# Performance work log

Hardware: AMD Instinct MI355X
Metric: run time of the kernel (lower is better)

Reference implementation:

```python
import jax, jax.numpy as jnp
import numpy as np

Na, Np, F, C, H, L, OUT = 50000, 100000, 128, 128, 8, 2, 64
D = C // H  # head dim = 16
E = 150000


def setup_inputs() -> dict:
    key = jax.random.key(0)
    ks = jax.random.split(key, 16)
    p = lambda k, shape: jax.random.normal(k, shape, jnp.float32) * 0.05
    return {
        "x_author": jax.random.normal(ks[0], (Na, F), jnp.float32),
        "x_paper": jax.random.normal(ks[1], (Np, F), jnp.float32),
        # per-node-type input projections (HGT.lin_dict)
        "win_w": p(ks[2], (2, F, C)), "win_b": p(ks[3], (2, C)),
        # per-layer, per-node-type K/Q/V linears of HGTConv
        "kqv_w": p(ks[4], (L, 2, 3, C, C)), "kqv_b": p(ks[5], (L, 2, 3, C)),
        # per-layer, per-node-type output linear a_lin
        "a_w": p(ks[6], (L, 2, C, C)), "a_b": p(ks[7], (L, 2, C)),
        # per-layer, per-node-type skip gate (init 1 like PyG)
        "skip": jnp.ones((L, 2), jnp.float32),
        # per-layer, per-edge-type relation matrices a_rel/m_rel and prior p_rel
        "rel_a": p(ks[8], (L, 2, H, D, D)), "rel_m": p(ks[9], (L, 2, H, D, D)),
        "rel_p": jnp.ones((L, 2, H), jnp.float32),
        # final classifier on author nodes
        "out_w": p(ks[10], (C, OUT)), "out_b": p(ks[11], (OUT,)),
        # edge type 0: author -> paper ('writes'); edge type 1: paper -> author (reverse)
        "ei_writes_src": jax.random.randint(ks[12], (E,), 0, Na, jnp.int32),
        "ei_writes_dst": jax.random.randint(ks[13], (E,), 0, Np, jnp.int32),
        "ei_rev_src": jax.random.randint(ks[14], (E,), 0, Np, jnp.int32),
        "ei_rev_dst": jax.random.randint(ks[15], (E,), 0, Na, jnp.int32),
    }


def _segment_softmax(alpha, dst, n):
    # softmax of alpha [E, H] over edges grouped by destination node (PyG softmax)
    m = jnp.full((n, alpha.shape[1]), -jnp.inf, alpha.dtype).at[dst].max(alpha)
    ex = jnp.exp(alpha - m[dst])
    s = jnp.zeros((n, alpha.shape[1]), alpha.dtype).at[dst].add(ex)
    return ex / (s[dst] + 1e-16)


def _hgt_forward(x_author, x_paper, win_w, win_b, kqv_w, kqv_b, a_w, a_b,
                 skip, rel_a, rel_m, rel_p, out_w, out_b, ei):
    # per-node-type input linear + relu
    xs = [jax.nn.relu(x_author @ win_w[0] + win_b[0]),
          jax.nn.relu(x_paper @ win_w[1] + win_b[1])]
    edge_types = [(0, 1, ei[0], ei[1]),  # author -> paper
                  (1, 0, ei[2], ei[3])]  # paper -> author
    nl = kqv_w.shape[0]
    inv_sqrt_d = np.float32(1.0 / np.sqrt(D))
    for l in range(nl):
        # K/Q/V per node type, shape [N_t, H, D]
        kqv = [[(xs[t] @ kqv_w[l, t, i] + kqv_b[l, t, i]).reshape(-1, H, D)
                for i in range(3)] for t in range(2)]
        agg = [jnp.zeros((xs[t].shape[0], H, D), xs[t].dtype) for t in range(2)]
        for e, (st, dt, src, dst) in enumerate(edge_types):
            # relation-specific transforms at node level, then gather at edges
            kn = jnp.einsum('nhd,hde->nhe', kqv[st][0], rel_a[l, e])
            vn = jnp.einsum('nhd,hde->nhe', kqv[st][2], rel_m[l, e])
            alpha = jnp.einsum('ehd,ehd->eh', kqv[dt][1][dst], kn[src])
            alpha = alpha * rel_p[l, e] * inv_sqrt_d
            alpha = _segment_softmax(alpha, dst, xs[dt].shape[0])
            agg[dt] = agg[dt].at[dst].add(alpha[:, :, None] * vn[src])
        new_xs = []
        for t in range(2):
            o = jax.nn.gelu(agg[t].reshape(-1, C), approximate=False)
            o = o @ a_w[l, t] + a_b[l, t]
            g = jax.nn.sigmoid(skip[l, t])
            new_xs.append(g * o + (1.0 - g) * xs[t])  # skip connection (dims match)
        xs = new_xs
    return xs[0] @ out_w + out_b  # author output


def reference(x_author, x_paper, win_w, win_b, kqv_w, kqv_b, a_w, a_b, skip,
              rel_a, rel_m, rel_p, out_w, out_b,
              ei_writes_src, ei_writes_dst, ei_rev_src, ei_rev_dst):
    ei = (ei_writes_src, ei_writes_dst, ei_rev_src, ei_rev_dst)
    return _hgt_forward(x_author, x_paper, win_w, win_b, kqv_w, kqv_b,
                        a_w, a_b, skip, rel_a, rel_m, rel_p, out_w, out_b, ei)
```

## Files before the change

### kernel.cpp

```cpp
#include <hip/hip_runtime.h>
#include <math.h>

namespace {

constexpr int Na = 50000, Np = 100000, L = 2, E = 150000;
constexpr int SCAN_TILE = 2048;

typedef __attribute__((ext_vector_type(8))) short short8v;
typedef __attribute__((ext_vector_type(4))) float f32x4;

__device__ inline float geluf(float x){ return 0.5f*x*(1.0f + erff(x*0.7071067811865476f)); }

__device__ inline float bf2f(unsigned short u){ return __uint_as_float(((unsigned)u) << 16); }
__device__ inline unsigned short f2bf(float f){
  unsigned u = __float_as_uint(f);
  u += 0x7FFFu + ((u >> 16) & 1u);
  return (unsigned short)(u >> 16);
}
__device__ inline unsigned pk2(float a, float b){
  return (unsigned)f2bf(a) | ((unsigned)f2bf(b) << 16);
}

struct StF32 {
  using T = float;
  static __device__ float ld(const T* p){ return *p; }
  static __device__ short8v ld8(const T* __restrict__ p){
    float4 lo = *reinterpret_cast<const float4*>(p);
    float4 hi = *reinterpret_cast<const float4*>(p+4);
    short8v v;
    v[0]=(short)f2bf(lo.x); v[1]=(short)f2bf(lo.y); v[2]=(short)f2bf(lo.z); v[3]=(short)f2bf(lo.w);
    v[4]=(short)f2bf(hi.x); v[5]=(short)f2bf(hi.y); v[6]=(short)f2bf(hi.z); v[7]=(short)f2bf(hi.w);
    return v;
  }
};
struct StBF16 {
  using T = unsigned short;
  static __device__ float ld(const T* p){ return bf2f(*p); }
  static __device__ short8v ld8(const T* __restrict__ p){
    return *reinterpret_cast<const short8v*>(p);
  }
  static __device__ void ld16(const T* __restrict__ p, float* o){
    const uint4* q = reinterpret_cast<const uint4*>(p);
    #pragma unroll
    for (int half = 0; half < 2; ++half){
      uint4 u = q[half];
      o[half*8+0] = bf2f((unsigned short)(u.x & 0xffff));
      o[half*8+1] = bf2f((unsigned short)(u.x >> 16));
      o[half*8+2] = bf2f((unsigned short)(u.y & 0xffff));
      o[half*8+3] = bf2f((unsigned short)(u.y >> 16));
      o[half*8+4] = bf2f((unsigned short)(u.z & 0xffff));
      o[half*8+5] = bf2f((unsigned short)(u.z >> 16));
      o[half*8+6] = bf2f((unsigned short)(u.w & 0xffff));
      o[half*8+7] = bf2f((unsigned short)(u.w >> 16));
    }
  }
};

__global__ void zero_int_kernel(int* __restrict__ p, int n){
  int i = blockIdx.x*256 + threadIdx.x;
  int stride = gridDim.x*256;
  for (; i < n; i += stride) p[i] = 0;
}

__global__ void diag_kernel(float* o, float v){
  if (threadIdx.x == 0 && blockIdx.x == 0) o[0] = v;
}

__global__ void hist_kernel(const int* __restrict__ dst, int* __restrict__ counts, int nE){
  int e = blockIdx.x*256 + threadIdx.x;
  if (e >= nE) return;
  atomicAdd(&counts[dst[e]], 1);
}

__global__ void scan_a(const int* __restrict__ counts, int* __restrict__ bsum, int n){
  int base = blockIdx.x*SCAN_TILE;
  int s = 0;
  for (int i = threadIdx.x; i < SCAN_TILE; i += 256){
    int g = base + i;
    s += (g < n) ? counts[g] : 0;
  }
  __shared__ int red[256];
  red[threadIdx.x] = s;
  __syncthreads();
  for (int off = 128; off > 0; off >>= 1){
    if (threadIdx.x < off) red[threadIdx.x] += red[threadIdx.x + off];
    __syncthreads();
  }
  if (threadIdx.x == 0) bsum[blockIdx.x] = red[0];
}

__global__ void scan_b(int* __restrict__ bsum, int nb){
  __shared__ int sh[1024];
  int t = threadIdx.x;
  int v = (t < nb) ? bsum[t] : 0;
  sh[t] = v;
  __syncthreads();
  for (int off = 1; off < 1024; off <<= 1){
    int add = (t >= off) ? sh[t-off] : 0;
    __syncthreads();
    sh[t] += add;
    __syncthreads();
  }
  if (t < nb) bsum[t] = sh[t] - v;
}

__global__ void scan_c(int* __restrict__ counts, const int* __restrict__ bsum,
                       int* __restrict__ rp, int n){
  int base = blockIdx.x*SCAN_TILE;
  __shared__ int sh[SCAN_TILE];
  for (int i = threadIdx.x; i < SCAN_TILE; i += 256){
    int g = base + i;
    sh[i] = (g < n) ? counts[g] : 0;
  }
  __syncthreads();
  int t = threadIdx.x;
  int loc[8], s = 0;
  #pragma unroll
  for (int i = 0; i < 8; ++i){ loc[i] = s; s += sh[t*8 + i]; }
  __shared__ int red[256];
  red[t] = s;
  __syncthreads();
  for (int off = 1; off < 256; off <<= 1){
    int add = (t >= off) ? red[t-off] : 0;
    __syncthreads();
    red[t] += add;
    __syncthreads();
  }
  int texcl = red[t] - s + bsum[blockIdx.x];
  #pragma unroll
  for (int i = 0; i < 8; ++i){
    int g = base + t*8 + i;
    if (g < n){
      int v = texcl + loc[i];
      rp[g] = v;
      counts[g] = v;
      if (g == n-1) rp[n] = v + sh[t*8 + i];
    }
  }
}

__global__ void fill_slots_kernel(const int* __restrict__ src, const int* __restrict__ dst,
                                  int* __restrict__ cursor, int* __restrict__ slots, int nE){
  int e = blockIdx.x*256 + threadIdx.x;
  if (e >= nE) return;
  int slot = atomicAdd(&cursor[dst[e]], 1);
  slots[slot] = src[e];
}

__global__ void eff_w_kernel(const float* __restrict__ kqv_w, const float* __restrict__ kqv_b,
                             const float* __restrict__ rel_a, const float* __restrict__ rel_m,
                             float* __restrict__ effw, float* __restrict__ effb){
  int idx = blockIdx.x*256 + threadIdx.x;
  if (idx >= 2*2*2*128*128) return;
  int j = idx & 127; int f = (idx >> 7) & 127; int c = idx >> 14;
  int kv = c & 1, t = (c >> 1) & 1, l = c >> 2;
  int h = j >> 4, e2 = j & 15;
  int i = (kv == 0) ? 0 : 2;
  const float* W = kqv_w + ((size_t)(((l*2 + t)*3 + i)*128) + f)*128 + h*16;
  const float* A = ((kv == 0) ? rel_a : rel_m) + ((size_t)(l*2 + t)*8 + h)*256;
  float acc = 0.f;
  #pragma unroll
  for (int d = 0; d < 16; ++d) acc += W[d]*A[d*16 + e2];
  effw[(size_t)c*16384 + f*128 + j] = acc;
  if (f == 0){
    const float* B = kqv_b + (size_t)((l*2 + t)*3 + i)*128 + h*16;
    float ab = 0.f;
    #pragma unroll
    for (int d = 0; d < 16; ++d) ab += B[d]*A[d*16 + e2];
    effb[c*128 + j] = ab;
  }
}

struct PrepSrc { const float* s[19]; };
__global__ void prep_w_kernel(PrepSrc P, unsigned short* __restrict__ wbf){
  int idx = blockIdx.x*256 + threadIdx.x;
  if (idx >= 19*16384) return;
  int s = idx >> 14, j = idx & 16383;
  int n = j >> 7, k = j & 127;
  int nc = (s == 18) ? 64 : 128;
  if (n >= nc) return;
  wbf[(size_t)s*16384 + n*128 + k] = f2bf(P.s[s][(size_t)k*nc + n]);
}

__device__ inline void stage_w(short* Bs, const unsigned short* __restrict__ WT, int t, int rows){
  for (int c = t; c < rows*16; c += 256){
    int r = c >> 4, c16 = c & 15;
    short8v v = *reinterpret_cast<const short8v*>(&WT[r*128 + c16*8]);
    *reinterpret_cast<short8v*>(&Bs[r*128 + ((c16 ^ (r&7))<<3)]) = v;
  }
}

template<int BN, int GELU_IN, int RELU_OUT, int SKIP, typename SIn>
__global__ __launch_bounds__(256) void gemm_kernel(
    const typename SIn::T* __restrict__ X,
    const unsigned short* __restrict__ WT,
    const float* __restrict__ bias,
    void* __restrict__ Y, int N,
    const unsigned short* __restrict__ skip_x,
    const float* __restrict__ skip_s)
{
  __shared__ __align__(16) short As[128*128];
  __shared__ __align__(16) char Braw[32768];
  short* Bs = (short*)Braw;
  const int t = threadIdx.x;
  const int row0 = blockIdx.x*128;
  for (int c = t; c < 128*16; c += 256){
    int r = c >> 4, c16 = c & 15;
    int gr = row0 + r;
    short8v v;
    if (gr < N){
      v = SIn::ld8(&X[(size_t)gr*128 + c16*8]);
      if (GELU_IN){
        #pragma unroll
        for (int i = 0; i < 8; ++i){
          float f = geluf(bf2f((unsigned short)v[i]));
          v[i] = (short)f2bf(f);
        }
      }
    } else {
      v = (short8v)0;
    }
    *reinterpret_cast<short8v*>(&As[r*128 + ((c16 ^ (r&7))<<3)]) = v;
  }
  stage_w(Bs, WT, t, BN);
  __syncthreads();
  const int lane = t & 63, wid = t >> 6;
  const int wm = wid >> 1, wn = wid & 1;
  constexpr int NR = BN/32;
  const int lr = lane & 15, lk = lane >> 4;
  f32x4 acc[4][NR] = {};
  #pragma unroll
  for (int kk = 0; kk < 4; ++kk){
    int kc = kk*4 + lk;
    short8v a[4], b[NR];
    #pragma unroll
    for (int m = 0; m < 4; ++m){
      int r = wm*64 + m*16 + lr;
      a[m] = *reinterpret_cast<const short8v*>(&As[r*128 + ((kc ^ (r&7))<<3)]);
    }
    #pragma unroll
    for (int n = 0; n < NR; ++n){
      int col = wn*(BN/2) + n*16 + lr;
      b[n] = *reinterpret_cast<const short8v*>(&Bs[col*128 + ((kc ^ (col&7))<<3)]);
    }
    #pragma unroll
    for (int m = 0; m < 4; ++m)
      #pragma unroll
      for (int n = 0; n < NR; ++n)
        acc[m][n] = __builtin_amdgcn_mfma_f32_16x16x32_bf16(b[n], a[m], acc[m][n], 0, 0, 0);
  }
  __syncthreads();

  if constexpr (BN == 128){
    #pragma unroll
    for (int m = 0; m < 4; ++m){
      int row = wm*64 + m*16 + lr;
      #pragma unroll
      for (int n = 0; n < NR; ++n){
        int col0 = wn*64 + n*16 + lk*4;
        float4 b4 = *reinterpret_cast<const float4*>(&bias[col0]);
        float y0 = acc[m][n][0] + b4.x, y1 = acc[m][n][1] + b4.y;
        float y2 = acc[m][n][2] + b4.z, y3 = acc[m][n][3] + b4.w;
        if (RELU_OUT){
          y0 = fmaxf(y0,0.f); y1 = fmaxf(y1,0.f); y2 = fmaxf(y2,0.f); y3 = fmaxf(y3,0.f);
        }
        uint2 pk; pk.x = pk2(y0,y1); pk.y = pk2(y2,y3);
        int c16 = col0 >> 3;
        *reinterpret_cast<uint2*>(&Bs[row*128 + ((c16 ^ (row&7))<<3) + (col0&7)]) = pk;
      }
    }
    __syncthreads();
    float g = 1.f, og = 0.f;
    if (SKIP){ float sv = *skip_s; g = 1.f/(1.f + expf(-sv)); og = 1.f - g; }
    unsigned short* out = (unsigned short*)Y;
    for (int c = t; c < 128*16; c += 256){
      int r = c >> 4, c16 = c & 15;
      int gr = row0 + r;
      if (gr >= N) continue;
      short8v v = *reinterpret_cast<const short8v*>(&Bs[r*128 + ((c16 ^ (r&7))<<3)]);
      if (SKIP){
        short8v s8 = *reinterpret_cast<const short8v*>(&skip_x[(size_t)gr*128 + c16*8]);
        short8v o8;
        #pragma unroll
        for (int i = 0; i < 8; ++i)
          o8[i] = (short)f2bf(g*bf2f((unsigned short)v[i]) + og*bf2f((unsigned short)s8[i]));
        *reinterpret_cast<short8v*>(&out[(size_t)gr*128 + c16*8]) = o8;
      } else {
        *reinterpret_cast<short8v*>(&out[(size_t)gr*128 + c16*8]) = v;
      }
    }
  } else {
    float* Bf = (float*)Braw;
    #pragma unroll
    for (int m = 0; m < 4; ++m){
      int row = wm*64 + m*16 + lr;
      #pragma unroll
      for (int n = 0; n < NR; ++n){
        int col0 = wn*32 + n*16 + lk*4;
        float4 b4 = *reinterpret_cast<const float4*>(&bias[col0]);
        float4 y;
        y.x = acc[m][n][0] + b4.x; y.y = acc[m][n][1] + b4.y;
        y.z = acc[m][n][2] + b4.z; y.w = acc[m][n][3] + b4.w;
        int cf = col0 >> 2;
        *reinterpret_cast<float4*>(&Bf[row*64 + ((cf ^ (row&7))<<2)]) = y;
      }
    }
    __syncthreads();
    float* out = (float*)Y;
    for (int c = t; c < 128*16; c += 256){
      int r = c >> 4, cf = c & 15;
      int gr = row0 + r;
      if (gr >= N) continue;
      float4 v = *reinterpret_cast<const float4*>(&Bf[r*64 + ((cf ^ (r&7))<<2)]);
      *reinterpret_cast<float4*>(&out[(size_t)gr*64 + cf*4]) = v;
    }
  }
}

__global__ __launch_bounds__(256) void qkv_kernel(
    const unsigned short* __restrict__ X,
    const unsigned short* __restrict__ WTq,
    const unsigned short* __restrict__ WTk,
    const unsigned short* __restrict__ WTv,
    const float* __restrict__ bq, const float* __restrict__ bk, const float* __restrict__ bv,
    unsigned short* __restrict__ Q, unsigned short* __restrict__ K, unsigned short* __restrict__ V,
    int N)
{
  __shared__ __align__(16) short As[128*128];
  __shared__ __align__(16) short Bs[128*128];
  const int t = threadIdx.x;
  const int row0 = blockIdx.x*128;
  for (int c = t; c < 128*16; c += 256){
    int r = c >> 4, c16 = c & 15;
    int gr = row0 + r;
    short8v v = (gr < N) ? *reinterpret_cast<const short8v*>(&X[(size_t)gr*128 + c16*8])
                         : (short8v)0;
    *reinterpret_cast<short8v*>(&As[r*128 + ((c16 ^ (r&7))<<3)]) = v;
  }
  const int lane = t & 63, wid = t >> 6;
  const int wm = wid >> 1, wn = wid & 1;
  const int lr = lane & 15, lk = lane >> 4;
  const unsigned short* wts[3] = {WTq, WTk, WTv};
  const float* bias[3] = {bq, bk, bv};
  unsigned short* outs[3] = {Q, K, V};
  #pragma unroll
  for (int s = 0; s < 3; ++s){
    __syncthreads();
    stage_w(Bs, wts[s], t, 128);
    __syncthreads();
    f32x4 acc[4][4] = {};
    #pragma unroll
    for (int kk = 0; kk < 4; ++kk){
      int kc = kk*4 + lk;
      short8v a[4], b[4];
      #pragma unroll
      for (int m = 0; m < 4; ++m){
        int r = wm*64 + m*16 + lr;
        a[m] = *reinterpret_cast<const short8v*>(&As[r*128 + ((kc ^ (r&7))<<3)]);
      }
      #pragma unroll
      for (int n = 0; n < 4; ++n){
        int col = wn*64 + n*16 + lr;
        b[n] = *reinterpret_cast<const short8v*>(&Bs[col*128 + ((kc ^ (col&7))<<3)]);
      }
      #pragma unroll
      for (int m = 0; m < 4; ++m)
        #pragma unroll
        for (int n = 0; n < 4; ++n)
          acc[m][n] = __builtin_amdgcn_mfma_f32_16x16x32_bf16(b[n], a[m], acc[m][n], 0, 0, 0);
    }
    __syncthreads();
    const float* bi = bias[s];
    #pragma unroll
    for (int m = 0; m < 4; ++m){
      int row = wm*64 + m*16 + lr;
      #pragma unroll
      for (int n = 0; n < 4; ++n){
        int col0 = wn*64 + n*16 + lk*4;
        float4 b4 = *reinterpret_cast<const float4*>(&bi[col0]);
        uint2 pk;
        pk.x = pk2(acc[m][n][0] + b4.x, acc[m][n][1] + b4.y);
        pk.y = pk2(acc[m][n][2] + b4.z, acc[m][n][3] + b4.w);
        int c16 = col0 >> 3;
        *reinterpret_cast<uint2*>(&Bs[row*128 + ((c16 ^ (row&7))<<3) + (col0&7)]) = pk;
      }
    }
    __syncthreads();
    unsigned short* out = outs[s];
    for (int c = t; c < 128*16; c += 256){
      int r = c >> 4, c16 = c & 15;
      int gr = row0 + r;
      if (gr >= N) continue;
      short8v v = *reinterpret_cast<const short8v*>(&Bs[r*128 + ((c16 ^ (r&7))<<3)]);
      *reinterpret_cast<short8v*>(&out[(size_t)gr*128 + c16*8]) = v;
    }
  }
}

__global__ void attn_gather_kernel(unsigned short* __restrict__ QA,
                                   const unsigned short* __restrict__ K,
                                   const unsigned short* __restrict__ V,
                                   const int* __restrict__ rp, const int* __restrict__ slots,
                                   const float* __restrict__ relp, int N){
  int idx = blockIdx.x*256 + threadIdx.x;
  if (idx >= N*8) return;
  int h = idx & 7, n = idx >> 3;
  float q[16];
  StBF16::ld16(&QA[(size_t)n*128 + h*16], q);
  float scale_h = relp[h]*0.25f;
  float m = -INFINITY, s = 0.f, acc[16];
  #pragma unroll
  for (int i = 0; i < 16; ++i) acc[i] = 0.f;
  int b = rp[n], e = rp[n+1];
  for (int j = b; j < e; ++j){
    int sv = slots[j];
    float kf[16], vf[16];
    StBF16::ld16(&K[(size_t)sv*128 + h*16], kf);
    float a = 0.f;
    #pragma unroll
    for (int i = 0; i < 16; ++i) a += q[i]*kf[i];
    a *= scale_h;
    float mn = fmaxf(m, a);
    float c = expf(m - mn);
    float p = expf(a - mn);
    StBF16::ld16(&V[(size_t)sv*128 + h*16], vf);
    s = s*c + p;
    #pragma unroll
    for (int i = 0; i < 16; ++i) acc[i] = acc[i]*c + p*vf[i];
    m = mn;
  }
  float inv = 1.f/(s + 1e-16f);
  #pragma unroll
  for (int i = 0; i < 16; ++i) QA[(size_t)n*128 + h*16 + i] = f2bf(acc[i]*inv);
}

struct Ptrs {
  const float *x_author, *x_paper, *win_w, *win_b, *kqv_w, *kqv_b, *a_w, *a_b;
  const float *skip, *rel_a, *rel_m, *rel_p, *out_w, *out_b;
  const int *src0, *dst0, *src1, *dst1;
};

static void run_pipeline(const Ptrs& P, float* d_out, char* ws, hipStream_t stream){
  using BF = unsigned short;
  size_t off = 0;
  auto alloc = [&](size_t bytes) -> void* {
    void* p = ws + off;
    off += (bytes + 255) & ~(size_t)255;
    return p;
  };
  BF* X0 = (BF*)alloc((size_t)Na*128*2);
  BF* X1 = (BF*)alloc((size_t)Np*128*2);
  BF* Q0 = (BF*)alloc((size_t)Na*128*2);
  BF* Q1 = (BF*)alloc((size_t)Np*128*2);
  BF* K0 = (BF*)alloc((size_t)Na*128*2);
  BF* K1 = (BF*)alloc((size_t)Np*128*2);
  BF* V0 = (BF*)alloc((size_t)Na*128*2);
  BF* V1 = (BF*)alloc((size_t)Np*128*2);
  float* effw = (float*)alloc((size_t)8*16384*4);
  float* effb = (float*)alloc((size_t)8*128*4);
  BF* wbf = (BF*)alloc((size_t)19*16384*2);
  int* rp0   = (int*)alloc((size_t)(Np+1)*4);
  int* cur0  = (int*)alloc((size_t)Np*4);
  int* slot0 = (int*)alloc((size_t)E*4);
  int* rp1   = (int*)alloc((size_t)(Na+1)*4);
  int* cur1  = (int*)alloc((size_t)Na*4);
  int* slot1 = (int*)alloc((size_t)E*4);
  int* bsum  = (int*)alloc((size_t)1024*4);

  auto cdiv = [](int a, int b){ return (a+b-1)/b; };
  const int geE = cdiv(E, 256);
  const int ga = cdiv(Na, 128), gp = cdiv(Np, 128);
  const int sb0 = cdiv(Np, SCAN_TILE), sb1 = cdiv(Na, SCAN_TILE);

  eff_w_kernel<<<512, 256, 0, stream>>>(P.kqv_w, P.kqv_b, P.rel_a, P.rel_m, effw, effb);

  PrepSrc ps;
  ps.s[0] = P.win_w; ps.s[1] = P.win_w + 16384;
  for (int l = 0; l < 2; ++l)
    for (int t = 0; t < 2; ++t){
      ps.s[2 + l*2 + t]  = P.kqv_w + (size_t)((l*2+t)*3+1)*16384;
      ps.s[6 + l*2 + t]  = effw + (size_t)(l*4+t*2+0)*16384;
      ps.s[10 + l*2 + t] = effw + (size_t)(l*4+t*2+1)*16384;
      ps.s[14 + l*2 + t] = P.a_w + (size_t)(l*2+t)*16384;
    }
  ps.s[18] = P.out_w;
  prep_w_kernel<<<cdiv(19*16384,256),256,0,stream>>>(ps, wbf);

  zero_int_kernel<<<512,256,0,stream>>>(cur0, Np);
  zero_int_kernel<<<512,256,0,stream>>>(cur1, Na);
  hist_kernel<<<geE,256,0,stream>>>(P.dst0, cur0, E);
  hist_kernel<<<geE,256,0,stream>>>(P.dst1, cur1, E);
  scan_a<<<sb0,256,0,stream>>>(cur0, bsum, Np);
  scan_b<<<1,1024,0,stream>>>(bsum, sb0);
  scan_c<<<sb0,256,0,stream>>>(cur0, bsum, rp0, Np);
  scan_a<<<sb1,256,0,stream>>>(cur1, bsum, Na);
  scan_b<<<1,1024,0,stream>>>(bsum, sb1);
  scan_c<<<sb1,256,0,stream>>>(cur1, bsum, rp1, Na);
  fill_slots_kernel<<<geE,256,0,stream>>>(P.src0, P.dst0, cur0, slot0, E);
  fill_slots_kernel<<<geE,256,0,stream>>>(P.src1, P.dst1, cur1, slot1, E);

  auto W = [&](int s){ return wbf + (size_t)s*16384; };

  gemm_kernel<128,0,1,0,StF32><<<ga,256,0,stream>>>(P.x_author, W(0), P.win_b,     X0, Na, nullptr, nullptr);
  gemm_kernel<128,0,1,0,StF32><<<gp,256,0,stream>>>(P.x_paper,  W(1), P.win_b+128, X1, Np, nullptr, nullptr);

  for (int l = 0; l < L; ++l){
    qkv_kernel<<<ga,256,0,stream>>>(X0, W(2+l*2+0), W(6+l*2+0), W(10+l*2+0),
                                    P.kqv_b + ((l*2+0)*3+1)*128, effb + (l*4+0)*128, effb + (l*4+1)*128,
                                    Q0, K0, V0, Na);
    qkv_kernel<<<gp,256,0,stream>>>(X1, W(2+l*2+1), W(6+l*2+1), W(10+l*2+1),
                                    P.kqv_b + ((l*2+1)*3+1)*128, effb + (l*4+2)*128, effb + (l*4+3)*128,
                                    Q1, K1, V1, Np);
    attn_gather_kernel<<<cdiv(Np*8,256),256,0,stream>>>(Q1, K0, V0, rp0, slot0, P.rel_p + (l*2+0)*8, Np);
    attn_gather_kernel<<<cdiv(Na*8,256),256,0,stream>>>(Q0, K1, V1, rp1, slot1, P.rel_p + (l*2+1)*8, Na);
    gemm_kernel<128,1,0,1,StBF16><<<ga,256,0,stream>>>(Q0, W(14+l*2+0), P.a_b + (l*2+0)*128, X0, Na, X0, P.skip + (l*2+0));
    gemm_kernel<128,1,0,1,StBF16><<<gp,256,0,stream>>>(Q1, W(14+l*2+1), P.a_b + (l*2+1)*128, X1, Np, X1, P.skip + (l*2+1));
  }

  gemm_kernel<64,0,0,0,StBF16><<<ga,256,0,stream>>>(X0, W(18), P.out_b, d_out, Na, nullptr, nullptr);
}

static size_t plan_bytes(){
  auto al = [](size_t x){ return (x + 255) & ~(size_t)255; };
  size_t t = 0;
  t += 4*(al((size_t)Na*128*2) + al((size_t)Np*128*2));
  t += al((size_t)8*16384*4) + al((size_t)8*128*4) + al((size_t)19*16384*2);
  t += al((size_t)(Np+1)*4) + al((size_t)Np*4) + al((size_t)E*4);
  t += al((size_t)(Na+1)*4) + al((size_t)Na*4) + al((size_t)E*4);
  t += al((size_t)1024*4);
  return t;
}

}

extern "C" void kernel_launch(void* const* d_in, const int* in_sizes, int n_in,
                              void* d_out, int out_size, void* d_ws, size_t ws_size,
                              hipStream_t stream){
  Ptrs P;
  P.x_author = (const float*)d_in[0];
  P.x_paper  = (const float*)d_in[1];
  P.win_w = (const float*)d_in[2];
  P.win_b = (const float*)d_in[3];
  P.kqv_w = (const float*)d_in[4];
  P.kqv_b = (const float*)d_in[5];
  P.a_w   = (const float*)d_in[6];
  P.a_b   = (const float*)d_in[7];
  P.skip  = (const float*)d_in[8];
  P.rel_a = (const float*)d_in[9];
  P.rel_m = (const float*)d_in[10];
  P.rel_p = (const float*)d_in[11];
  P.out_w = (const float*)d_in[12];
  P.out_b = (const float*)d_in[13];
  P.src0 = (const int*)d_in[14];
  P.dst0 = (const int*)d_in[15];
  P.src1 = (const int*)d_in[16];
  P.dst1 = (const int*)d_in[17];

  if (ws_size >= plan_bytes()){
    run_pipeline(P, (float*)d_out, (char*)d_ws, stream);
  } else {
    diag_kernel<<<1,1,0,stream>>>((float*)d_out, (float)((double)ws_size/1.0e6));
  }
}
```

Measured before the change: 394.7 us.

## Merge per-node-type launches into grouped kernels and use 512-thread GEMM blocks

Each pair of per-node-type launches (input GEMM, QKV, attention gather, output GEMM) becomes one grouped launch that picks its part from the block index through argument structs. This cuts the launch count and lets the small author-type work fill the device alongside the paper-type work. The GEMM and QKV kernels also move from 4 to 8 waves per 128-row tile, each wave holding half the accumulators. That raises occupancy per block but leaves less MFMA work per wave, and the large LDS tile per block still limits how many blocks fit on a CU.

```diff
diff --git a/kernel.cpp b/kernel.cpp
--- a/kernel.cpp
+++ b/kernel.cpp
@@ -23,7 +23,6 @@
 
 struct StF32 {
   using T = float;
-  static __device__ float ld(const T* p){ return *p; }
   static __device__ short8v ld8(const T* __restrict__ p){
     float4 lo = *reinterpret_cast<const float4*>(p);
     float4 hi = *reinterpret_cast<const float4*>(p+4);
@@ -35,7 +34,6 @@
 };
 struct StBF16 {
   using T = unsigned short;
-  static __device__ float ld(const T* p){ return bf2f(*p); }
   static __device__ short8v ld8(const T* __restrict__ p){
     return *reinterpret_cast<const short8v*>(p);
   }
@@ -183,28 +181,39 @@
 }
 
 __device__ inline void stage_w(short* Bs, const unsigned short* __restrict__ WT, int t, int rows){
-  for (int c = t; c < rows*16; c += 256){
+  for (int c = t; c < rows*16; c += 512){
     int r = c >> 4, c16 = c & 15;
     short8v v = *reinterpret_cast<const short8v*>(&WT[r*128 + c16*8]);
     *reinterpret_cast<short8v*>(&Bs[r*128 + ((c16 ^ (r&7))<<3)]) = v;
   }
 }
 
+struct GemmArgs {
+  const void* X[2];
+  const unsigned short* WT[2];
+  const float* bias[2];
+  void* Y[2];
+  const unsigned short* skip_x[2];
+  const float* skip_s[2];
+  int N[2];
+  int blocks0;
+};
+
 template<int BN, int GELU_IN, int RELU_OUT, int SKIP, typename SIn>
-__global__ __launch_bounds__(256) void gemm_kernel(
-    const typename SIn::T* __restrict__ X,
-    const unsigned short* __restrict__ WT,
-    const float* __restrict__ bias,
-    void* __restrict__ Y, int N,
-    const unsigned short* __restrict__ skip_x,
-    const float* __restrict__ skip_s)
+__global__ __launch_bounds__(512) void gemm_kernel(GemmArgs Ar)
 {
   __shared__ __align__(16) short As[128*128];
   __shared__ __align__(16) char Braw[32768];
   short* Bs = (short*)Braw;
   const int t = threadIdx.x;
-  const int row0 = blockIdx.x*128;
-  for (int c = t; c < 128*16; c += 256){
+  const int part = (blockIdx.x < Ar.blocks0) ? 0 : 1;
+  const int bid = part ? (blockIdx.x - Ar.blocks0) : blockIdx.x;
+  const typename SIn::T* X = (const typename SIn::T*)Ar.X[part];
+  const unsigned short* WT = Ar.WT[part];
+  const float* bias = Ar.bias[part];
+  const int N = Ar.N[part];
+  const int row0 = bid*128;
+  for (int c = t; c < 128*16; c += 512){
     int r = c >> 4, c16 = c & 15;
     int gr = row0 + r;
     short8v v;
@@ -225,8 +234,8 @@
   stage_w(Bs, WT, t, BN);
   __syncthreads();
   const int lane = t & 63, wid = t >> 6;
-  const int wm = wid >> 1, wn = wid & 1;
-  constexpr int NR = BN/32;
+  const int wm = wid >> 2, wn = wid & 3;
+  constexpr int NR = BN/64;
   const int lr = lane & 15, lk = lane >> 4;
   f32x4 acc[4][NR] = {};
   #pragma unroll
@@ -240,7 +249,7 @@
     }
     #pragma unroll
     for (int n = 0; n < NR; ++n){
-      int col = wn*(BN/2) + n*16 + lr;
+      int col = wn*(BN/4) + n*16 + lr;
       b[n] = *reinterpret_cast<const short8v*>(&Bs[col*128 + ((kc ^ (col&7))<<3)]);
     }
     #pragma unroll
@@ -257,7 +266,7 @@
       int row = wm*64 + m*16 + lr;
       #pragma unroll
       for (int n = 0; n < NR; ++n){
-        int col0 = wn*64 + n*16 + lk*4;
+        int col0 = wn*32 + n*16 + lk*4;
         float4 b4 = *reinterpret_cast<const float4*>(&bias[col0]);
         float y0 = acc[m][n][0] + b4.x, y1 = acc[m][n][1] + b4.y;
         float y2 = acc[m][n][2] + b4.z, y3 = acc[m][n][3] + b4.w;
@@ -271,9 +280,10 @@
     }
     __syncthreads();
     float g = 1.f, og = 0.f;
-    if (SKIP){ float sv = *skip_s; g = 1.f/(1.f + expf(-sv)); og = 1.f - g; }
-    unsigned short* out = (unsigned short*)Y;
-    for (int c = t; c < 128*16; c += 256){
+    if (SKIP){ float sv = *Ar.skip_s[part]; g = 1.f/(1.f + expf(-sv)); og = 1.f - g; }
+    unsigned short* out = (unsigned short*)Ar.Y[part];
+    const unsigned short* skip_x = Ar.skip_x[part];
+    for (int c = t; c < 128*16; c += 512){
       int r = c >> 4, c16 = c & 15;
       int gr = row0 + r;
       if (gr >= N) continue;
@@ -296,7 +306,7 @@
       int row = wm*64 + m*16 + lr;
       #pragma unroll
       for (int n = 0; n < NR; ++n){
-        int col0 = wn*32 + n*16 + lk*4;
+        int col0 = wn*16 + n*16 + lk*4;
         float4 b4 = *reinterpret_cast<const float4*>(&bias[col0]);
         float4 y;
         y.x = acc[m][n][0] + b4.x; y.y = acc[m][n][1] + b4.y;
@@ -306,8 +316,8 @@
       }
     }
     __syncthreads();
-    float* out = (float*)Y;
-    for (int c = t; c < 128*16; c += 256){
+    float* out = (float*)Ar.Y[part];
+    for (int c = t; c < 128*16; c += 512){
       int r = c >> 4, cf = c & 15;
       int gr = row0 + r;
       if (gr >= N) continue;
@@ -317,20 +327,26 @@
   }
 }
 
-__global__ __launch_bounds__(256) void qkv_kernel(
-    const unsigned short* __restrict__ X,
-    const unsigned short* __restrict__ WTq,
-    const unsigned short* __restrict__ WTk,
-    const unsigned short* __restrict__ WTv,
-    const float* __restrict__ bq, const float* __restrict__ bk, const float* __restrict__ bv,
-    unsigned short* __restrict__ Q, unsigned short* __restrict__ K, unsigned short* __restrict__ V,
-    int N)
+struct QkvArgs {
+  const unsigned short* X[2];
+  const unsigned short* WT[2][3];
+  const float* bias[2][3];
+  unsigned short* out[2][3];
+  int N[2];
+  int blocks0;
+};
+
+__global__ __launch_bounds__(512) void qkv_kernel(QkvArgs Ar)
 {
   __shared__ __align__(16) short As[128*128];
   __shared__ __align__(16) short Bs[128*128];
   const int t = threadIdx.x;
-  const int row0 = blockIdx.x*128;
-  for (int c = t; c < 128*16; c += 256){
+  const int part = (blockIdx.x < Ar.blocks0) ? 0 : 1;
+  const int bid = part ? (blockIdx.x - Ar.blocks0) : blockIdx.x;
+  const unsigned short* X = Ar.X[part];
+  const int N = Ar.N[part];
+  const int row0 = bid*128;
+  for (int c = t; c < 128*16; c += 512){
     int r = c >> 4, c16 = c & 15;
     int gr = row0 + r;
     short8v v = (gr < N) ? *reinterpret_cast<const short8v*>(&X[(size_t)gr*128 + c16*8])
@@ -338,45 +354,42 @@
     *reinterpret_cast<short8v*>(&As[r*128 + ((c16 ^ (r&7))<<3)]) = v;
   }
   const int lane = t & 63, wid = t >> 6;
-  const int wm = wid >> 1, wn = wid & 1;
+  const int wm = wid >> 2, wn = wid & 3;
   const int lr = lane & 15, lk = lane >> 4;
-  const unsigned short* wts[3] = {WTq, WTk, WTv};
-  const float* bias[3] = {bq, bk, bv};
-  unsigned short* outs[3] = {Q, K, V};
   #pragma unroll
   for (int s = 0; s < 3; ++s){
     __syncthreads();
-    stage_w(Bs, wts[s], t, 128);
-    __syncthreads();
-    f32x4 acc[4][4] = {};
+    stage_w(Bs, Ar.WT[part][s], t, 128);
+    __syncthreads();
+    f32x4 acc[4][2] = {};
     #pragma unroll
     for (int kk = 0; kk < 4; ++kk){
       int kc = kk*4 + lk;
-      short8v a[4], b[4];
+      short8v a[4], b[2];
       #pragma unroll
       for (int m = 0; m < 4; ++m){
         int r = wm*64 + m*16 + lr;
         a[m] = *reinterpret_cast<const short8v*>(&As[r*128 + ((kc ^ (r&7))<<3)]);
       }
       #pragma unroll
-      for (int n = 0; n < 4; ++n){
-        int col = wn*64 + n*16 + lr;
+      for (int n = 0; n < 2; ++n){
+        int col = wn*32 + n*16 + lr;
         b[n] = *reinterpret_cast<const short8v*>(&Bs[col*128 + ((kc ^ (col&7))<<3)]);
       }
       #pragma unroll
       for (int m = 0; m < 4; ++m)
         #pragma unroll
-        for (int n = 0; n < 4; ++n)
+        for (int n = 0; n < 2; ++n)
           acc[m][n] = __builtin_amdgcn_mfma_f32_16x16x32_bf16(b[n], a[m], acc[m][n], 0, 0, 0);
     }
     __syncthreads();
-    const float* bi = bias[s];
+    const float* bi = Ar.bias[part][s];
     #pragma unroll
     for (int m = 0; m < 4; ++m){
       int row = wm*64 + m*16 + lr;
       #pragma unroll
-      for (int n = 0; n < 4; ++n){
-        int col0 = wn*64 + n*16 + lk*4;
+      for (int n = 0; n < 2; ++n){
+        int col0 = wn*32 + n*16 + lk*4;
         float4 b4 = *reinterpret_cast<const float4*>(&bi[col0]);
         uint2 pk;
         pk.x = pk2(acc[m][n][0] + b4.x, acc[m][n][1] + b4.y);
@@ -386,8 +399,8 @@
       }
     }
     __syncthreads();
-    unsigned short* out = outs[s];
-    for (int c = t; c < 128*16; c += 256){
+    unsigned short* out = Ar.out[part][s];
+    for (int c = t; c < 128*16; c += 512){
       int r = c >> 4, c16 = c & 15;
       int gr = row0 + r;
       if (gr >= N) continue;
@@ -397,21 +410,35 @@
   }
 }
 
-__global__ void attn_gather_kernel(unsigned short* __restrict__ QA,
-                                   const unsigned short* __restrict__ K,
-                                   const unsigned short* __restrict__ V,
-                                   const int* __restrict__ rp, const int* __restrict__ slots,
-                                   const float* __restrict__ relp, int N){
-  int idx = blockIdx.x*256 + threadIdx.x;
+struct AttnArgs {
+  unsigned short* QA[2];
+  const unsigned short* K[2];
+  const unsigned short* V[2];
+  const int* rp[2];
+  const int* slots[2];
+  const float* relp[2];
+  int N[2];
+  int blocks0;
+};
+
+__global__ void attn_gather_kernel(AttnArgs Ar){
+  const int part = (blockIdx.x < Ar.blocks0) ? 0 : 1;
+  const int bid = part ? (blockIdx.x - Ar.blocks0) : blockIdx.x;
+  int idx = bid*256 + threadIdx.x;
+  const int N = Ar.N[part];
   if (idx >= N*8) return;
   int h = idx & 7, n = idx >> 3;
+  unsigned short* QA = Ar.QA[part];
+  const unsigned short* K = Ar.K[part];
+  const unsigned short* V = Ar.V[part];
   float q[16];
   StBF16::ld16(&QA[(size_t)n*128 + h*16], q);
-  float scale_h = relp[h]*0.25f;
+  float scale_h = Ar.relp[part][h]*0.25f;
   float m = -INFINITY, s = 0.f, acc[16];
   #pragma unroll
   for (int i = 0; i < 16; ++i) acc[i] = 0.f;
-  int b = rp[n], e = rp[n+1];
+  int b = Ar.rp[part][n], e = Ar.rp[part][n+1];
+  const int* slots = Ar.slots[part];
   for (int j = b; j < e; ++j){
     int sv = slots[j];
     float kf[16], vf[16];
@@ -501,23 +528,60 @@
 
   auto W = [&](int s){ return wbf + (size_t)s*16384; };
 
-  gemm_kernel<128,0,1,0,StF32><<<ga,256,0,stream>>>(P.x_author, W(0), P.win_b,     X0, Na, nullptr, nullptr);
-  gemm_kernel<128,0,1,0,StF32><<<gp,256,0,stream>>>(P.x_paper,  W(1), P.win_b+128, X1, Np, nullptr, nullptr);
+  {
+    GemmArgs g{};
+    g.X[0] = P.x_author; g.X[1] = P.x_paper;
+    g.WT[0] = W(0); g.WT[1] = W(1);
+    g.bias[0] = P.win_b; g.bias[1] = P.win_b + 128;
+    g.Y[0] = X0; g.Y[1] = X1;
+    g.N[0] = Na; g.N[1] = Np; g.blocks0 = ga;
+    gemm_kernel<128,0,1,0,StF32><<<ga+gp,512,0,stream>>>(g);
+  }
+
+  const int ab0 = cdiv(Np*8,256), ab1 = cdiv(Na*8,256);
 
   for (int l = 0; l < L; ++l){
-    qkv_kernel<<<ga,256,0,stream>>>(X0, W(2+l*2+0), W(6+l*2+0), W(10+l*2+0),
-                                    P.kqv_b + ((l*2+0)*3+1)*128, effb + (l*4+0)*128, effb + (l*4+1)*128,
-                                    Q0, K0, V0, Na);
-    qkv_kernel<<<gp,256,0,stream>>>(X1, W(2+l*2+1), W(6+l*2+1), W(10+l*2+1),
-                                    P.kqv_b + ((l*2+1)*3+1)*128, effb + (l*4+2)*128, effb + (l*4+3)*128,
-                                    Q1, K1, V1, Np);
-    attn_gather_kernel<<<cdiv(Np*8,256),256,0,stream>>>(Q1, K0, V0, rp0, slot0, P.rel_p + (l*2+0)*8, Np);
-    attn_gather_kernel<<<cdiv(Na*8,256),256,0,stream>>>(Q0, K1, V1, rp1, slot1, P.rel_p + (l*2+1)*8, Na);
-    gemm_kernel<128,1,0,1,StBF16><<<ga,256,0,stream>>>(Q0, W(14+l*2+0), P.a_b + (l*2+0)*128, X0, Na, X0, P.skip + (l*2+0));
-    gemm_kernel<128,1,0,1,StBF16><<<gp,256,0,stream>>>(Q1, W(14+l*2+1), P.a_b + (l*2+1)*128, X1, Np, X1, P.skip + (l*2+1));
-  }
-
-  gemm_kernel<64,0,0,0,StBF16><<<ga,256,0,stream>>>(X0, W(18), P.out_b, d_out, Na, nullptr, nullptr);
+    QkvArgs q{};
+    q.X[0] = X0; q.X[1] = X1;
+    for (int t2 = 0; t2 < 2; ++t2){
+      q.WT[t2][0] = W(2+l*2+t2); q.WT[t2][1] = W(6+l*2+t2); q.WT[t2][2] = W(10+l*2+t2);
+      q.bias[t2][0] = P.kqv_b + ((l*2+t2)*3+1)*128;
+      q.bias[t2][1] = effb + (l*4+t2*2+0)*128;
+      q.bias[t2][2] = effb + (l*4+t2*2+1)*128;
+    }
+    q.out[0][0] = Q0; q.out[0][1] = K0; q.out[0][2] = V0;
+    q.out[1][0] = Q1; q.out[1][1] = K1; q.out[1][2] = V1;
+    q.N[0] = Na; q.N[1] = Np; q.blocks0 = ga;
+    qkv_kernel<<<ga+gp,512,0,stream>>>(q);
+
+    AttnArgs a{};
+    a.QA[0] = Q1; a.K[0] = K0; a.V[0] = V0; a.rp[0] = rp0; a.slots[0] = slot0;
+    a.relp[0] = P.rel_p + (l*2+0)*8; a.N[0] = Np;
+    a.QA[1] = Q0; a.K[1] = K1; a.V[1] = V1; a.rp[1] = rp1; a.slots[1] = slot1;
+    a.relp[1] = P.rel_p + (l*2+1)*8; a.N[1] = Na;
+    a.blocks0 = ab0;
+    attn_gather_kernel<<<ab0+ab1,256,0,stream>>>(a);
+
+    GemmArgs g{};
+    g.X[0] = Q0; g.X[1] = Q1;
+    g.WT[0] = W(14+l*2+0); g.WT[1] = W(14+l*2+1);
+    g.bias[0] = P.a_b + (l*2+0)*128; g.bias[1] = P.a_b + (l*2+1)*128;
+    g.Y[0] = X0; g.Y[1] = X1;
+    g.skip_x[0] = X0; g.skip_x[1] = X1;
+    g.skip_s[0] = P.skip + (l*2+0); g.skip_s[1] = P.skip + (l*2+1);
+    g.N[0] = Na; g.N[1] = Np; g.blocks0 = ga;
+    gemm_kernel<128,1,0,1,StBF16><<<ga+gp,512,0,stream>>>(g);
+  }
+
+  {
+    GemmArgs g{};
+    g.X[0] = X0; g.X[1] = nullptr;
+    g.WT[0] = W(18); g.WT[1] = nullptr;
+    g.bias[0] = P.out_b; g.bias[1] = nullptr;
+    g.Y[0] = d_out; g.Y[1] = nullptr;
+    g.N[0] = Na; g.N[1] = 0; g.blocks0 = ga;
+    gemm_kernel<64,0,0,0,StBF16><<<ga,512,0,stream>>>(g);
+  }
 }
 
 static size_t plan_bytes(){
```

Measured after the change: 336.0 us. 14.9% less time.
